# Kernel optimization log

Hardware: AMD Instinct MI355X
Metric: run time of the kernel (lower is better)

The kernel has to match this reference:

```python
import jax, jax.numpy as jnp
import numpy as np

K = 3
ALPHA = 8.3

def _patches(x, oh, ow):
    # x: [B, C, H, W] -> [B, C, K, K, oh, ow] (stride=1, dilation=1)
    rows = []
    for k in range(K):
        cols = [x[:, :, k:k + oh, l:l + ow] for l in range(K)]
        rows.append(jnp.stack(cols, axis=2))  # [B, C, K, oh, ow]
    return jnp.stack(rows, axis=2)  # [B, C, K, K, oh, ow]

def setup_inputs() -> dict:
    key = jax.random.key(0)
    k1, k2, k3, k4 = jax.random.split(key, 4)
    B, C, H, W = 4, 64, 256, 256
    OC = 64
    img = jax.random.normal(k1, (B, C, H, W), dtype=jnp.float32)
    depth = jax.random.uniform(k2, (B, 1, H, W), dtype=jnp.float32)
    weight = jax.random.uniform(k3, (OC, C, K, K), dtype=jnp.float32, minval=-0.1, maxval=0.1)
    bias = jax.random.uniform(k4, (1, OC), dtype=jnp.float32, minval=-0.1, maxval=0.1)
    return {"img": img, "depth": depth, "weight": weight, "bias": bias}

def reference(img, depth, weight, bias):
    B, C, H, W = img.shape
    oh, ow = H - K + 1, W - K + 1
    c0 = K // 2
    img_p = _patches(img, oh, ow)                 # [B, C, K, K, oh, ow]
    dep_p = _patches(depth, oh, ow)[:, 0]         # [B, K, K, oh, ow]
    center = depth[:, 0, c0:c0 + oh, c0:c0 + ow]  # [B, oh, ow]
    dw = jnp.exp(-ALPHA * jnp.abs(dep_p - center[:, None, None]))  # [B, K, K, oh, ow]
    out = jnp.einsum('bcklpq,bklpq,ockl->bopq', img_p, dw, weight)
    out = out + bias[0][None, :, None, None]
    return out
```

## Files before the change

kernel.cpp:

```cpp
#include <hip/hip_runtime.h>
#include <hip/hip_bf16.h>

typedef __bf16 bf16_t;
typedef __bf16 bf16x4 __attribute__((ext_vector_type(4)));
typedef __bf16 bf16x8 __attribute__((ext_vector_type(8)));
typedef float f32x4 __attribute__((ext_vector_type(4)));

#define ALPHA 8.3f
#define CPAD 72
#define NCOL 68


__global__ void repack_w(const float* __restrict__ w, bf16_t* __restrict__ w2) {
    int idx = blockIdx.x * 256 + threadIdx.x;
    if (idx >= 9 * 2 * 4 * 64 * 8) return;
    int j     = idx & 7;
    int lane  = (idx >> 3) & 63;
    int m     = (idx >> 9) & 3;
    int chunk = (idx >> 11) & 1;
    int tap   = idx >> 12;
    int oc = m * 16 + (lane & 15);
    int c  = chunk * 32 + (lane >> 4) * 8 + j;
    int kt = tap / 3, lt = tap % 3;
    w2[idx] = (bf16_t)w[((oc * 64 + c) * 3 + kt) * 3 + lt];
}

__global__ __launch_bounds__(256, 2) void depthconv_mfma(
    const float* __restrict__ img, const float* __restrict__ depth,
    const bf16_t* __restrict__ w2, const float* __restrict__ bias,
    float* __restrict__ out)
{
    __shared__ bf16_t lds[4 * NCOL * CPAD];

    const int tid = threadIdx.x;
    const int blk   = blockIdx.x;
    const int ppair = blk >> 4;
    const int r     = blk & 15;
    const int b     = r >> 2;
    const int qt    = r & 3;
    const int p0    = ppair * 2;
    const int q0    = (qt == 3) ? 190 : qt * 64;
    const int s0    = (qt == 3) ? 188 : q0;

    const float* imgb = img + (size_t)b * 64 * 65536;
    const float* dep  = depth + (size_t)b * 65536;

#pragma unroll
    for (int k = 0; k < 5; ++k) {
        int u = tid + (k << 8);
        if (u < 1088) {
            int cg   = u & 15;
            int rest = u >> 4;
            int colg = rest % 17;
            int row  = rest / 17;
            const float* src = imgb + (size_t)(cg * 4) * 65536 + (p0 + row) * 256 + s0 + colg * 4;
            f32x4 v0 = *(const f32x4*)src;
            f32x4 v1 = *(const f32x4*)(src + 65536);
            f32x4 v2 = *(const f32x4*)(src + 2 * 65536);
            f32x4 v3 = *(const f32x4*)(src + 3 * 65536);
            bf16_t* dst = lds + (size_t)(row * NCOL + colg * 4) * CPAD + cg * 4;
#pragma unroll
            for (int i = 0; i < 4; ++i)
                *(bf16x4*)(dst + i * CPAD) =
                    (bf16x4){(bf16_t)v0[i], (bf16_t)v1[i], (bf16_t)v2[i], (bf16_t)v3[i]};
        }
    }
    __syncthreads();

    const int wv   = tid >> 6;
    const int lane = tid & 63;
    const int pr   = wv >> 1;
    const int mh   = wv & 1;
    const int n    = lane & 15;
    const int quad = lane >> 4;
    const int prow = p0 + pr;
    const int clb0 = q0 - s0;

    float dc[4];
#pragma unroll
    for (int i = 0; i < 4; ++i)
        dc[i] = dep[(prow + 1) * 256 + q0 + 16 * i + n + 1];

    const f32x4 Z = (f32x4){0.f, 0.f, 0.f, 0.f};
    f32x4 acc[2][4];
#pragma unroll
    for (int mm = 0; mm < 2; ++mm)
#pragma unroll
        for (int i = 0; i < 4; ++i) acc[mm][i] = Z;

    for (int kt = 0; kt < 3; ++kt) {
        float dwv[3][4];
#pragma unroll
        for (int lt = 0; lt < 3; ++lt)
#pragma unroll
            for (int i = 0; i < 4; ++i) {
                float d = dep[(prow + kt) * 256 + q0 + 16 * i + n + lt];
                dwv[lt][i] = __expf(-ALPHA * fabsf(d - dc[i]));
            }
#pragma unroll
        for (int lt = 0; lt < 3; ++lt) {
            const int tap = kt * 3 + lt;
            const bf16x8* w2p = (const bf16x8*)w2 + ((size_t)(tap * 2) * 4 + mh * 2) * 64 + lane;
            bf16x8 a00 = w2p[0];
            bf16x8 a01 = w2p[64];
            bf16x8 a10 = w2p[256];
            bf16x8 a11 = w2p[256 + 64];
#pragma unroll
            for (int i = 0; i < 4; ++i) {
                const bf16_t* lp = lds
                    + (size_t)((pr + kt) * NCOL + clb0 + 16 * i + n + lt) * CPAD + quad * 8;
                const bf16x8 bf0 = *(const bf16x8*)lp;
                const bf16x8 bf1 = *(const bf16x8*)(lp + 32);
                f32x4 P0 = __builtin_amdgcn_mfma_f32_16x16x32_bf16(a00, bf0, Z, 0, 0, 0);
                f32x4 P1 = __builtin_amdgcn_mfma_f32_16x16x32_bf16(a01, bf0, Z, 0, 0, 0);
                P0 = __builtin_amdgcn_mfma_f32_16x16x32_bf16(a10, bf1, P0, 0, 0, 0);
                P1 = __builtin_amdgcn_mfma_f32_16x16x32_bf16(a11, bf1, P1, 0, 0, 0);
                acc[0][i] += dwv[lt][i] * P0;
                acc[1][i] += dwv[lt][i] * P1;
            }
        }
    }

#pragma unroll
    for (int mm = 0; mm < 2; ++mm) {
#pragma unroll
        for (int r2 = 0; r2 < 4; ++r2) {
            int oc = (mh * 2 + mm) * 16 + quad * 4 + r2;
            float bz = bias[oc];
#pragma unroll
            for (int i = 0; i < 4; ++i) {
                int q = q0 + 16 * i + n;
                out[((size_t)(b * 64 + oc) * 254 + prow) * 254 + q] = acc[mm][i][r2] + bz;
            }
        }
    }
}

extern "C" void kernel_launch(void* const* d_in, const int* in_sizes, int n_in,
                              void* d_out, int out_size, void* d_ws, size_t ws_size,
                              hipStream_t stream) {
    const float* img   = (const float*)d_in[0];
    const float* depth = (const float*)d_in[1];
    const float* w     = (const float*)d_in[2];
    const float* bias  = (const float*)d_in[3];
    bf16_t* w2 = (bf16_t*)d_ws;

    repack_w<<<144, 256, 0, stream>>>(w, w2);
    depthconv_mfma<<<2032, 256, 0, stream>>>(img, depth, w2, bias, (float*)d_out);
}
```

Measured before the change: 152.0 us.

## Process four output rows per block with a rolling LDS row buffer and prefetch

Each block now computes four output rows in two passes instead of two, reusing the two overlapping input rows held in LDS as a ring of row slots, and loads only the two new rows for the second pass. The global loads for those two rows are issued before the first pass's compute so their latency overlaps the MFMA work. This cuts the redundant halo reads of the image and halves the grid. In exchange it holds extra prefetch registers, which may hurt occupancy, adds two block barriers, and leaves fewer blocks to spread across CUs.

```diff
diff --git a/kernel.cpp b/kernel.cpp
--- a/kernel.cpp
+++ b/kernel.cpp
@@ -32,13 +32,13 @@
 {
     __shared__ bf16_t lds[4 * NCOL * CPAD];
 
-    const int tid = threadIdx.x;
+    const int tid   = threadIdx.x;
     const int blk   = blockIdx.x;
-    const int ppair = blk >> 4;
+    const int strip = blk >> 4;
     const int r     = blk & 15;
     const int b     = r >> 2;
     const int qt    = r & 3;
-    const int p0    = ppair * 2;
+    const int p0    = (strip == 63) ? 250 : strip * 4;
     const int q0    = (qt == 3) ? 190 : qt * 64;
     const int s0    = (qt == 3) ? 188 : q0;
 
@@ -67,71 +67,121 @@
     }
     __syncthreads();
 
+    const int pcg   = tid & 15;
+    const int pcolg = tid >> 4;
+    const float* psrc = imgb + (size_t)(pcg * 4) * 65536 + (p0 + 4) * 256 + s0 + pcolg * 4;
+    f32x4 pf[4][2];
+#pragma unroll
+    for (int ch = 0; ch < 4; ++ch)
+#pragma unroll
+        for (int rw = 0; rw < 2; ++rw)
+            pf[ch][rw] = *(const f32x4*)(psrc + (size_t)ch * 65536 + rw * 256);
+
     const int wv   = tid >> 6;
     const int lane = tid & 63;
     const int pr   = wv >> 1;
     const int mh   = wv & 1;
     const int n    = lane & 15;
     const int quad = lane >> 4;
-    const int prow = p0 + pr;
     const int clb0 = q0 - s0;
 
-    float dc[4];
-#pragma unroll
-    for (int i = 0; i < 4; ++i)
-        dc[i] = dep[(prow + 1) * 256 + q0 + 16 * i + n + 1];
-
     const f32x4 Z = (f32x4){0.f, 0.f, 0.f, 0.f};
-    f32x4 acc[2][4];
-#pragma unroll
-    for (int mm = 0; mm < 2; ++mm)
-#pragma unroll
-        for (int i = 0; i < 4; ++i) acc[mm][i] = Z;
-
-    for (int kt = 0; kt < 3; ++kt) {
-        float dwv[3][4];
-#pragma unroll
-        for (int lt = 0; lt < 3; ++lt)
-#pragma unroll
-            for (int i = 0; i < 4; ++i) {
-                float d = dep[(prow + kt) * 256 + q0 + 16 * i + n + lt];
-                dwv[lt][i] = __expf(-ALPHA * fabsf(d - dc[i]));
-            }
-#pragma unroll
-        for (int lt = 0; lt < 3; ++lt) {
-            const int tap = kt * 3 + lt;
-            const bf16x8* w2p = (const bf16x8*)w2 + ((size_t)(tap * 2) * 4 + mh * 2) * 64 + lane;
-            bf16x8 a00 = w2p[0];
-            bf16x8 a01 = w2p[64];
-            bf16x8 a10 = w2p[256];
-            bf16x8 a11 = w2p[256 + 64];
-#pragma unroll
-            for (int i = 0; i < 4; ++i) {
-                const bf16_t* lp = lds
-                    + (size_t)((pr + kt) * NCOL + clb0 + 16 * i + n + lt) * CPAD + quad * 8;
-                const bf16x8 bf0 = *(const bf16x8*)lp;
-                const bf16x8 bf1 = *(const bf16x8*)(lp + 32);
-                f32x4 P0 = __builtin_amdgcn_mfma_f32_16x16x32_bf16(a00, bf0, Z, 0, 0, 0);
-                f32x4 P1 = __builtin_amdgcn_mfma_f32_16x16x32_bf16(a01, bf0, Z, 0, 0, 0);
-                P0 = __builtin_amdgcn_mfma_f32_16x16x32_bf16(a10, bf1, P0, 0, 0, 0);
-                P1 = __builtin_amdgcn_mfma_f32_16x16x32_bf16(a11, bf1, P1, 0, 0, 0);
-                acc[0][i] += dwv[lt][i] * P0;
-                acc[1][i] += dwv[lt][i] * P1;
-            }
-        }
-    }
-
-#pragma unroll
-    for (int mm = 0; mm < 2; ++mm) {
-#pragma unroll
-        for (int r2 = 0; r2 < 4; ++r2) {
-            int oc = (mh * 2 + mm) * 16 + quad * 4 + r2;
-            float bz = bias[oc];
-#pragma unroll
-            for (int i = 0; i < 4; ++i) {
-                int q = q0 + 16 * i + n;
-                out[((size_t)(b * 64 + oc) * 254 + prow) * 254 + q] = acc[mm][i][r2] + bz;
-            }
+
+#pragma unroll
+    for (int t = 0; t < 2; ++t) {
+        const int prow = p0 + 2 * t + pr;
+        const int sb   = 2 * t;
+
+        float dc[4];
+#pragma unroll
+        for (int i = 0; i < 4; ++i)
+            dc[i] = dep[(prow + 1) * 256 + q0 + 16 * i + n + 1];
+
+        f32x4 acc[2][4];
+#pragma unroll
+        for (int mm = 0; mm < 2; ++mm)
+#pragma unroll
+            for (int i = 0; i < 4; ++i) acc[mm][i] = Z;
+
+#pragma unroll
+        for (int kt = 0; kt < 3; ++kt) {
+            const int slot = (sb + pr + kt) & 3;
+            float dwv[3][4];
+#pragma unroll
+            for (int lt = 0; lt < 3; ++lt)
+#pragma unroll
+                for (int i = 0; i < 4; ++i) {
+                    float d = dep[(prow + kt) * 256 + q0 + 16 * i + n + lt];
+                    dwv[lt][i] = __expf(-ALPHA * fabsf(d - dc[i]));
+                }
+#pragma unroll
+            for (int lt = 0; lt < 3; ++lt) {
+                const int tap = kt * 3 + lt;
+                const bf16x8* w2p = (const bf16x8*)w2 + ((size_t)(tap * 2) * 4 + mh * 2) * 64 + lane;
+                bf16x8 a00 = w2p[0];
+                bf16x8 a01 = w2p[64];
+                bf16x8 a10 = w2p[256];
+                bf16x8 a11 = w2p[256 + 64];
+#pragma unroll
+                for (int i = 0; i < 4; ++i) {
+                    const bf16_t* lp = lds
+                        + (size_t)(slot * NCOL + clb0 + 16 * i + n + lt) * CPAD + quad * 8;
+                    const bf16x8 bf0 = *(const bf16x8*)lp;
+                    const bf16x8 bf1 = *(const bf16x8*)(lp + 32);
+                    f32x4 P0 = __builtin_amdgcn_mfma_f32_16x16x32_bf16(a00, bf0, Z, 0, 0, 0);
+                    f32x4 P1 = __builtin_amdgcn_mfma_f32_16x16x32_bf16(a01, bf0, Z, 0, 0, 0);
+                    P0 = __builtin_amdgcn_mfma_f32_16x16x32_bf16(a10, bf1, P0, 0, 0, 0);
+                    P1 = __builtin_amdgcn_mfma_f32_16x16x32_bf16(a11, bf1, P1, 0, 0, 0);
+                    acc[0][i] += dwv[lt][i] * P0;
+                    acc[1][i] += dwv[lt][i] * P1;
+                }
+            }
+        }
+
+#pragma unroll
+        for (int mm = 0; mm < 2; ++mm) {
+#pragma unroll
+            for (int r2 = 0; r2 < 4; ++r2) {
+                int oc = (mh * 2 + mm) * 16 + quad * 4 + r2;
+                float bz = bias[oc];
+#pragma unroll
+                for (int i = 0; i < 4; ++i) {
+                    int q = q0 + 16 * i + n;
+                    out[((size_t)(b * 64 + oc) * 254 + prow) * 254 + q] = acc[mm][i][r2] + bz;
+                }
+            }
+        }
+
+        if (t == 0) {
+            __syncthreads();
+
+            f32x4 tl[4];
+            const int trw = tid >> 4;
+            const float* tsrc = imgb + (size_t)(pcg * 4) * 65536 + (p0 + 4 + trw) * 256 + s0 + 64;
+            if (tid < 32) {
+#pragma unroll
+                for (int ch = 0; ch < 4; ++ch)
+                    tl[ch] = *(const f32x4*)(tsrc + (size_t)ch * 65536);
+            }
+
+#pragma unroll
+            for (int rw = 0; rw < 2; ++rw) {
+                bf16_t* dst = lds + (size_t)(rw * NCOL + pcolg * 4) * CPAD + pcg * 4;
+#pragma unroll
+                for (int i = 0; i < 4; ++i)
+                    *(bf16x4*)(dst + i * CPAD) =
+                        (bf16x4){(bf16_t)pf[0][rw][i], (bf16_t)pf[1][rw][i],
+                                 (bf16_t)pf[2][rw][i], (bf16_t)pf[3][rw][i]};
+            }
+            if (tid < 32) {
+                bf16_t* dst = lds + (size_t)(trw * NCOL + 64) * CPAD + pcg * 4;
+#pragma unroll
+                for (int i = 0; i < 4; ++i)
+                    *(bf16x4*)(dst + i * CPAD) =
+                        (bf16x4){(bf16_t)tl[0][i], (bf16_t)tl[1][i],
+                                 (bf16_t)tl[2][i], (bf16_t)tl[3][i]};
+            }
+            __syncthreads();
         }
     }
 }
@@ -146,5 +196,5 @@
     bf16_t* w2 = (bf16_t*)d_ws;
 
     repack_w<<<144, 256, 0, stream>>>(w, w2);
-    depthconv_mfma<<<2032, 256, 0, stream>>>(img, depth, w2, bias, (float*)d_out);
+    depthconv_mfma<<<1024, 256, 0, stream>>>(img, depth, w2, bias, (float*)d_out);
 }
```

New measurement: 153.8 us. About the same (+1.2%).

## Batch global loads before LDS stores and prefetch weights per tap

Applied to the files above, without the earlier changes.

The image tile is now loaded into registers all at once, with all 20 float4 loads issued before any bf16 conversion or LDS store, and the depth loads plus exp weights are computed before the barrier. This gives more memory-level parallelism and overlaps latency. The tap loop is fully unrolled, and the weight fragments for the next tap are prefetched from global memory while the current tap runs. The cost is higher register pressure from 64+ staged floats and 36 depth weights, which could spill or reduce occupancy under launch_bounds(256,2).

```diff
diff --git a/kernel.cpp b/kernel.cpp
--- a/kernel.cpp
+++ b/kernel.cpp
@@ -45,28 +45,6 @@
     const float* imgb = img + (size_t)b * 64 * 65536;
     const float* dep  = depth + (size_t)b * 65536;
 
-#pragma unroll
-    for (int k = 0; k < 5; ++k) {
-        int u = tid + (k << 8);
-        if (u < 1088) {
-            int cg   = u & 15;
-            int rest = u >> 4;
-            int colg = rest % 17;
-            int row  = rest / 17;
-            const float* src = imgb + (size_t)(cg * 4) * 65536 + (p0 + row) * 256 + s0 + colg * 4;
-            f32x4 v0 = *(const f32x4*)src;
-            f32x4 v1 = *(const f32x4*)(src + 65536);
-            f32x4 v2 = *(const f32x4*)(src + 2 * 65536);
-            f32x4 v3 = *(const f32x4*)(src + 3 * 65536);
-            bf16_t* dst = lds + (size_t)(row * NCOL + colg * 4) * CPAD + cg * 4;
-#pragma unroll
-            for (int i = 0; i < 4; ++i)
-                *(bf16x4*)(dst + i * CPAD) =
-                    (bf16x4){(bf16_t)v0[i], (bf16_t)v1[i], (bf16_t)v2[i], (bf16_t)v3[i]};
-        }
-    }
-    __syncthreads();
-
     const int wv   = tid >> 6;
     const int lane = tid & 63;
     const int pr   = wv >> 1;
@@ -76,10 +54,75 @@
     const int prow = p0 + pr;
     const int clb0 = q0 - s0;
 
-    float dc[4];
+    f32x4 v[4][4];
 #pragma unroll
-    for (int i = 0; i < 4; ++i)
-        dc[i] = dep[(prow + 1) * 256 + q0 + 16 * i + n + 1];
+    for (int k = 0; k < 4; ++k) {
+        const int u = tid + (k << 8);
+        const int cg = u & 15, rest = u >> 4;
+        const int colg = rest % 17, row = rest / 17;
+        const float* src = imgb + (size_t)(cg * 4) * 65536 + (p0 + row) * 256 + s0 + colg * 4;
+#pragma unroll
+        for (int ch = 0; ch < 4; ++ch)
+            v[k][ch] = *(const f32x4*)(src + (size_t)ch * 65536);
+    }
+    f32x4 tv[4];
+    {
+        const int u = 1024 + tid;
+        const int cg = u & 15, rest = u >> 4;
+        const int colg = rest % 17, row = rest / 17;
+        const float* src = imgb + (size_t)(cg * 4) * 65536 + (p0 + row) * 256 + s0 + colg * 4;
+        if (tid < 64) {
+#pragma unroll
+            for (int ch = 0; ch < 4; ++ch)
+                tv[ch] = *(const f32x4*)(src + (size_t)ch * 65536);
+        }
+    }
+
+    float dre[3][3][4];
+#pragma unroll
+    for (int kt = 0; kt < 3; ++kt)
+#pragma unroll
+        for (int lt = 0; lt < 3; ++lt)
+#pragma unroll
+            for (int i = 0; i < 4; ++i)
+                dre[kt][lt][i] = dep[(prow + kt) * 256 + q0 + 16 * i + n + lt];
+
+#pragma unroll
+    for (int k = 0; k < 4; ++k) {
+        const int u = tid + (k << 8);
+        const int cg = u & 15, rest = u >> 4;
+        const int colg = rest % 17, row = rest / 17;
+        bf16_t* dst = lds + (size_t)(row * NCOL + colg * 4) * CPAD + cg * 4;
+#pragma unroll
+        for (int i = 0; i < 4; ++i)
+            *(bf16x4*)(dst + i * CPAD) =
+                (bf16x4){(bf16_t)v[k][0][i], (bf16_t)v[k][1][i],
+                         (bf16_t)v[k][2][i], (bf16_t)v[k][3][i]};
+    }
+    if (tid < 64) {
+        const int u = 1024 + tid;
+        const int cg = u & 15, rest = u >> 4;
+        const int colg = rest % 17, row = rest / 17;
+        bf16_t* dst = lds + (size_t)(row * NCOL + colg * 4) * CPAD + cg * 4;
+#pragma unroll
+        for (int i = 0; i < 4; ++i)
+            *(bf16x4*)(dst + i * CPAD) =
+                (bf16x4){(bf16_t)tv[0][i], (bf16_t)tv[1][i],
+                         (bf16_t)tv[2][i], (bf16_t)tv[3][i]};
+    }
+
+    float dwv[3][3][4];
+#pragma unroll
+    for (int i = 0; i < 4; ++i) {
+        const float dc = dre[1][1][i];
+#pragma unroll
+        for (int kt = 0; kt < 3; ++kt)
+#pragma unroll
+            for (int lt = 0; lt < 3; ++lt)
+                dwv[kt][lt][i] = __expf(-ALPHA * fabsf(dre[kt][lt][i] - dc));
+    }
+
+    __syncthreads();
 
     const f32x4 Z = (f32x4){0.f, 0.f, 0.f, 0.f};
     f32x4 acc[2][4];
@@ -88,36 +131,29 @@
 #pragma unroll
         for (int i = 0; i < 4; ++i) acc[mm][i] = Z;
 
-    for (int kt = 0; kt < 3; ++kt) {
-        float dwv[3][4];
+    const bf16x8* wbase = (const bf16x8*)w2 + (size_t)(mh * 2) * 64 + lane;
+    bf16x8 c0 = wbase[0], c1 = wbase[64], c2 = wbase[256], c3 = wbase[320];
+
 #pragma unroll
-        for (int lt = 0; lt < 3; ++lt)
+    for (int tap = 0; tap < 9; ++tap) {
+        const int kt = tap / 3, lt = tap % 3;
+        const bf16x8 a00 = c0, a01 = c1, a10 = c2, a11 = c3;
+        if (tap < 8) {
+            const bf16x8* np = wbase + (size_t)(tap + 1) * 512;
+            c0 = np[0]; c1 = np[64]; c2 = np[256]; c3 = np[320];
+        }
 #pragma unroll
-            for (int i = 0; i < 4; ++i) {
-                float d = dep[(prow + kt) * 256 + q0 + 16 * i + n + lt];
-                dwv[lt][i] = __expf(-ALPHA * fabsf(d - dc[i]));
-            }
-#pragma unroll
-        for (int lt = 0; lt < 3; ++lt) {
-            const int tap = kt * 3 + lt;
-            const bf16x8* w2p = (const bf16x8*)w2 + ((size_t)(tap * 2) * 4 + mh * 2) * 64 + lane;
-            bf16x8 a00 = w2p[0];
-            bf16x8 a01 = w2p[64];
-            bf16x8 a10 = w2p[256];
-            bf16x8 a11 = w2p[256 + 64];
-#pragma unroll
-            for (int i = 0; i < 4; ++i) {
-                const bf16_t* lp = lds
-                    + (size_t)((pr + kt) * NCOL + clb0 + 16 * i + n + lt) * CPAD + quad * 8;
-                const bf16x8 bf0 = *(const bf16x8*)lp;
-                const bf16x8 bf1 = *(const bf16x8*)(lp + 32);
-                f32x4 P0 = __builtin_amdgcn_mfma_f32_16x16x32_bf16(a00, bf0, Z, 0, 0, 0);
-                f32x4 P1 = __builtin_amdgcn_mfma_f32_16x16x32_bf16(a01, bf0, Z, 0, 0, 0);
-                P0 = __builtin_amdgcn_mfma_f32_16x16x32_bf16(a10, bf1, P0, 0, 0, 0);
-                P1 = __builtin_amdgcn_mfma_f32_16x16x32_bf16(a11, bf1, P1, 0, 0, 0);
-                acc[0][i] += dwv[lt][i] * P0;
-                acc[1][i] += dwv[lt][i] * P1;
-            }
+        for (int i = 0; i < 4; ++i) {
+            const bf16_t* lp = lds
+                + (size_t)((pr + kt) * NCOL + clb0 + 16 * i + n + lt) * CPAD + quad * 8;
+            const bf16x8 bf0 = *(const bf16x8*)lp;
+            const bf16x8 bf1 = *(const bf16x8*)(lp + 32);
+            f32x4 P0 = __builtin_amdgcn_mfma_f32_16x16x32_bf16(a00, bf0, Z, 0, 0, 0);
+            f32x4 P1 = __builtin_amdgcn_mfma_f32_16x16x32_bf16(a01, bf0, Z, 0, 0, 0);
+            P0 = __builtin_amdgcn_mfma_f32_16x16x32_bf16(a10, bf1, P0, 0, 0, 0);
+            P1 = __builtin_amdgcn_mfma_f32_16x16x32_bf16(a11, bf1, P1, 0, 0, 0);
+            acc[0][i] += dwv[kt][lt][i] * P0;
+            acc[1][i] += dwv[kt][lt][i] * P1;
         }
     }
 
```

Result: slower. 155.5 us (+2.3%).

## Process four output rows per block with rolling LDS row buffer and prefetch

Applied to the files above, without the earlier changes.

Each block now computes a strip of four output rows instead of two. It keeps a 4-slot ring of input rows in LDS, prefetching the next image row into registers while the MFMA work for the current row runs. This cuts the redundant halo reloads of input rows and hides global load latency behind compute. Each wave now owns 16 output channels instead of splitting by row. The cost is higher register pressure from the prefetch buffers and depth values, fewer blocks in the grid, and an overlapping last strip that recomputes some rows.

```diff
diff --git a/kernel.cpp b/kernel.cpp
--- a/kernel.cpp
+++ b/kernel.cpp
@@ -33,107 +33,142 @@
     __shared__ bf16_t lds[4 * NCOL * CPAD];
 
     const int tid = threadIdx.x;
-    const int blk   = blockIdx.x;
-    const int ppair = blk >> 4;
+    const int blk = blockIdx.x;
+    const int strip = blk >> 4;
     const int r     = blk & 15;
     const int b     = r >> 2;
     const int qt    = r & 3;
-    const int p0    = ppair * 2;
+    const int pbase = (strip == 63) ? 250 : strip * 4;
     const int q0    = (qt == 3) ? 190 : qt * 64;
     const int s0    = (qt == 3) ? 188 : q0;
+    const int clb0  = q0 - s0;
 
     const float* imgb = img + (size_t)b * 64 * 65536;
     const float* dep  = depth + (size_t)b * 65536;
 
+    const int wv   = tid >> 6;
+    const int lane = tid & 63;
+    const int n    = lane & 15;
+    const int quad = lane >> 4;
+    const int cg   = tid & 15;
+    const int colg = tid >> 4;
+    const int hch  = wv * 16 + n;
+    const bool hact = (lane < 16);
+
+    const f32x4 Z = (f32x4){0.f, 0.f, 0.f, 0.f};
+
+#define LOAD_ROW(rowL, m, h)                                                              \
+    do {                                                                                  \
+        const float* _s = imgb + (size_t)(cg * 4) * 65536 + (size_t)(rowL) * 256 + s0 + colg * 4; \
+        m[0] = *(const f32x4*)_s;                                                         \
+        m[1] = *(const f32x4*)(_s + 65536);                                               \
+        m[2] = *(const f32x4*)(_s + 2 * 65536);                                           \
+        m[3] = *(const f32x4*)(_s + 3 * 65536);                                           \
+        if (hact) h = *(const f32x4*)(imgb + (size_t)hch * 65536 + (size_t)(rowL) * 256 + s0 + 64); \
+    } while (0)
+
+#define CVT_WRITE(slot, m, h)                                                             \
+    do {                                                                                  \
+        bf16_t* _d = lds + ((size_t)(slot) * NCOL + colg * 4) * CPAD + cg * 4;            \
+        _Pragma("unroll")                                                                 \
+        for (int _i = 0; _i < 4; ++_i)                                                    \
+            *(bf16x4*)(_d + _i * CPAD) = (bf16x4){(bf16_t)m[0][_i], (bf16_t)m[1][_i],     \
+                                                  (bf16_t)m[2][_i], (bf16_t)m[3][_i]};    \
+        if (hact) {                                                                       \
+            bf16_t* _hd = lds + ((size_t)(slot) * NCOL + 64) * CPAD + hch;                \
+            _Pragma("unroll")                                                             \
+            for (int _i = 0; _i < 4; ++_i) _hd[_i * CPAD] = (bf16_t)h[_i];                \
+        }                                                                                 \
+    } while (0)
+
+#define LOAD_DEP(prow)                                                                    \
+    do {                                                                                  \
+        _Pragma("unroll") for (int _kt = 0; _kt < 3; ++_kt)                               \
+        _Pragma("unroll") for (int _lt = 0; _lt < 3; ++_lt)                               \
+        _Pragma("unroll") for (int _i = 0; _i < 4; ++_i)                                  \
+            dre[_kt][_lt][_i] = dep[(size_t)((prow) + _kt) * 256 + q0 + 16 * _i + n + _lt]; \
+    } while (0)
+
+    f32x4 ma[4]; f32x4 hA = Z;
+    f32x4 mb[4]; f32x4 hB = Z;
+    LOAD_ROW(pbase + 0, ma, hA);
+    LOAD_ROW(pbase + 1, mb, hB);
+    CVT_WRITE(0, ma, hA);
+    CVT_WRITE(1, mb, hB);
+    LOAD_ROW(pbase + 2, ma, hA);
+    float dre[3][3][4];
+    LOAD_DEP(pbase);
+    f32x4 pm[4]; f32x4 ph = Z;
+    LOAD_ROW(pbase + 3, pm, ph);
+    CVT_WRITE(2, ma, hA);
+    asm volatile("s_waitcnt lgkmcnt(0)" ::: "memory");
+    __builtin_amdgcn_s_barrier();
+
+    const bf16x8* wbase = (const bf16x8*)w2 + (size_t)wv * 64 + lane;
+    float bz[4];
 #pragma unroll
-    for (int k = 0; k < 5; ++k) {
-        int u = tid + (k << 8);
-        if (u < 1088) {
-            int cg   = u & 15;
-            int rest = u >> 4;
-            int colg = rest % 17;
-            int row  = rest / 17;
-            const float* src = imgb + (size_t)(cg * 4) * 65536 + (p0 + row) * 256 + s0 + colg * 4;
-            f32x4 v0 = *(const f32x4*)src;
-            f32x4 v1 = *(const f32x4*)(src + 65536);
-            f32x4 v2 = *(const f32x4*)(src + 2 * 65536);
-            f32x4 v3 = *(const f32x4*)(src + 3 * 65536);
-            bf16_t* dst = lds + (size_t)(row * NCOL + colg * 4) * CPAD + cg * 4;
+    for (int r2 = 0; r2 < 4; ++r2) bz[r2] = bias[wv * 16 + quad * 4 + r2];
+
+#pragma unroll
+    for (int t = 0; t < 4; ++t) {
+        const int p = pbase + t;
+
+        float dwv[3][3][4];
+#pragma unroll
+        for (int i = 0; i < 4; ++i) {
+            const float dc = dre[1][1][i];
+#pragma unroll
+            for (int kt = 0; kt < 3; ++kt)
+#pragma unroll
+                for (int lt = 0; lt < 3; ++lt)
+                    dwv[kt][lt][i] = __expf(-ALPHA * fabsf(dre[kt][lt][i] - dc));
+        }
+
+        f32x4 acc[4];
+#pragma unroll
+        for (int i = 0; i < 4; ++i) acc[i] = Z;
+
+#pragma unroll
+        for (int kt = 0; kt < 3; ++kt) {
+            const int slot = (t + kt) & 3;
+#pragma unroll
+            for (int lt = 0; lt < 3; ++lt) {
+                const int tap = kt * 3 + lt;
+                const bf16x8 a0 = wbase[(size_t)(tap * 2 + 0) * 256];
+                const bf16x8 a1 = wbase[(size_t)(tap * 2 + 1) * 256];
+#pragma unroll
+                for (int i = 0; i < 4; ++i) {
+                    const bf16_t* lp = lds
+                        + ((size_t)slot * NCOL + clb0 + 16 * i + n + lt) * CPAD + quad * 8;
+                    const bf16x8 bf0 = *(const bf16x8*)lp;
+                    const bf16x8 bf1 = *(const bf16x8*)(lp + 32);
+                    f32x4 P = __builtin_amdgcn_mfma_f32_16x16x32_bf16(a0, bf0, Z, 0, 0, 0);
+                    P = __builtin_amdgcn_mfma_f32_16x16x32_bf16(a1, bf1, P, 0, 0, 0);
+                    acc[i] += dwv[kt][lt][i] * P;
+                }
+            }
+        }
+
+        if (t < 3) {
+            LOAD_DEP(p + 1);
+            CVT_WRITE((t + 3) & 3, pm, ph);
+            if (t < 2) LOAD_ROW(pbase + t + 4, pm, ph);
+            asm volatile("s_waitcnt lgkmcnt(0)" ::: "memory");
+            __builtin_amdgcn_s_barrier();
+        }
+
+#pragma unroll
+        for (int r2 = 0; r2 < 4; ++r2) {
+            const int oc = wv * 16 + quad * 4 + r2;
 #pragma unroll
             for (int i = 0; i < 4; ++i)
-                *(bf16x4*)(dst + i * CPAD) =
-                    (bf16x4){(bf16_t)v0[i], (bf16_t)v1[i], (bf16_t)v2[i], (bf16_t)v3[i]};
+                out[((size_t)(b * 64 + oc) * 254 + p) * 254 + q0 + 16 * i + n]
+                    = acc[i][r2] + bz[r2];
         }
     }
-    __syncthreads();
-
-    const int wv   = tid >> 6;
-    const int lane = tid & 63;
-    const int pr   = wv >> 1;
-    const int mh   = wv & 1;
-    const int n    = lane & 15;
-    const int quad = lane >> 4;
-    const int prow = p0 + pr;
-    const int clb0 = q0 - s0;
-
-    float dc[4];
-#pragma unroll
-    for (int i = 0; i < 4; ++i)
-        dc[i] = dep[(prow + 1) * 256 + q0 + 16 * i + n + 1];
-
-    const f32x4 Z = (f32x4){0.f, 0.f, 0.f, 0.f};
-    f32x4 acc[2][4];
-#pragma unroll
-    for (int mm = 0; mm < 2; ++mm)
-#pragma unroll
-        for (int i = 0; i < 4; ++i) acc[mm][i] = Z;
-
-    for (int kt = 0; kt < 3; ++kt) {
-        float dwv[3][4];
-#pragma unroll
-        for (int lt = 0; lt < 3; ++lt)
-#pragma unroll
-            for (int i = 0; i < 4; ++i) {
-                float d = dep[(prow + kt) * 256 + q0 + 16 * i + n + lt];
-                dwv[lt][i] = __expf(-ALPHA * fabsf(d - dc[i]));
-            }
-#pragma unroll
-        for (int lt = 0; lt < 3; ++lt) {
-            const int tap = kt * 3 + lt;
-            const bf16x8* w2p = (const bf16x8*)w2 + ((size_t)(tap * 2) * 4 + mh * 2) * 64 + lane;
-            bf16x8 a00 = w2p[0];
-            bf16x8 a01 = w2p[64];
-            bf16x8 a10 = w2p[256];
-            bf16x8 a11 = w2p[256 + 64];
-#pragma unroll
-            for (int i = 0; i < 4; ++i) {
-                const bf16_t* lp = lds
-                    + (size_t)((pr + kt) * NCOL + clb0 + 16 * i + n + lt) * CPAD + quad * 8;
-                const bf16x8 bf0 = *(const bf16x8*)lp;
-                const bf16x8 bf1 = *(const bf16x8*)(lp + 32);
-                f32x4 P0 = __builtin_amdgcn_mfma_f32_16x16x32_bf16(a00, bf0, Z, 0, 0, 0);
-                f32x4 P1 = __builtin_amdgcn_mfma_f32_16x16x32_bf16(a01, bf0, Z, 0, 0, 0);
-                P0 = __builtin_amdgcn_mfma_f32_16x16x32_bf16(a10, bf1, P0, 0, 0, 0);
-                P1 = __builtin_amdgcn_mfma_f32_16x16x32_bf16(a11, bf1, P1, 0, 0, 0);
-                acc[0][i] += dwv[lt][i] * P0;
-                acc[1][i] += dwv[lt][i] * P1;
-            }
-        }
-    }
-
-#pragma unroll
-    for (int mm = 0; mm < 2; ++mm) {
-#pragma unroll
-        for (int r2 = 0; r2 < 4; ++r2) {
-            int oc = (mh * 2 + mm) * 16 + quad * 4 + r2;
-            float bz = bias[oc];
-#pragma unroll
-            for (int i = 0; i < 4; ++i) {
-                int q = q0 + 16 * i + n;
-                out[((size_t)(b * 64 + oc) * 254 + prow) * 254 + q] = acc[mm][i][r2] + bz;
-            }
-        }
-    }
+#undef LOAD_ROW
+#undef CVT_WRITE
+#undef LOAD_DEP
 }
 
 extern "C" void kernel_launch(void* const* d_in, const int* in_sizes, int n_in,
@@ -146,5 +181,5 @@
     bf16_t* w2 = (bf16_t*)d_ws;
 
     repack_w<<<144, 256, 0, stream>>>(w, w2);
-    depthconv_mfma<<<2032, 256, 0, stream>>>(img, depth, w2, bias, (float*)d_out);
+    depthconv_mfma<<<1024, 256, 0, stream>>>(img, depth, w2, bias, (float*)d_out);
 }
```

Result: slower. 223.5 us (+47.0%).
